# Kernel tuning notes

Hardware: AMD Instinct MI355X
Metric: run time of the kernel (lower is better)

## Reference

```python
import jax, jax.numpy as jnp
import numpy as np
import math

B, S, D = 1, 4096, 1024
H, DK = 16, 64
WINDOW = 256
GLOBAL = 16


def setup_inputs() -> dict:
    key = jax.random.key(0)
    ks = jax.random.split(key, 8)
    scale = 1.0 / math.sqrt(D)  # xavier-ish scale for projections
    return {
        "query": jax.random.normal(ks[0], (B, S, D), jnp.float32),
        "key": jax.random.normal(ks[1], (B, S, D), jnp.float32),
        "value": jax.random.normal(ks[2], (B, S, D), jnp.float32),
        "Wq": jax.random.normal(ks[3], (D, D), jnp.float32) * scale,
        "bq": jnp.zeros((D,), jnp.float32),
        "Wk": jax.random.normal(ks[4], (D, D), jnp.float32) * scale,
        "bk": jnp.zeros((D,), jnp.float32),
        "Wv": jax.random.normal(ks[5], (D, D), jnp.float32) * scale,
        "bv": jnp.zeros((D,), jnp.float32),
        "Wo": jax.random.normal(ks[6], (D, D), jnp.float32) * scale,
        "bo": jnp.zeros((D,), jnp.float32),
    }


def _split_heads(x):
    # [B, S, D] -> [B, H, S, DK]
    return x.reshape(B, S, H, DK).transpose(0, 2, 1, 3)


def reference(query, key, value, Wq, bq, Wk, bk, Wv, bv, Wo, bo):
    Q = _split_heads(query @ Wq + bq)   # [B,H,S,DK]
    K = _split_heads(key @ Wk + bk)
    V = _split_heads(value @ Wv + bv)

    scores = jnp.einsum("bhqd,bhkd->bhqk", Q, K) / math.sqrt(DK)  # [B,H,S,S]

    i = jnp.arange(S)[:, None]
    j = jnp.arange(S)[None, :]
    local = jnp.abs(i - j) <= WINDOW
    glob = (i < GLOBAL) | (j < GLOBAL)
    causal = j <= i
    mask = (local | glob) & causal  # [S,S]

    scores = jnp.where(mask[None, None], scores, -jnp.inf)
    probs = jax.nn.softmax(scores, axis=-1)  # dropout is identity (p=0 / eval)

    out = jnp.einsum("bhqk,bhkd->bhqd", probs, V)  # [B,H,S,DK]
    out = out.transpose(0, 2, 1, 3).reshape(B, S, D)
    return out @ Wo + bo
```

## Files before the change

### kernel.cpp

```cpp
#include <hip/hip_runtime.h>

typedef __bf16 bf16_t;
typedef __attribute__((ext_vector_type(8))) __bf16 bf16x8;
typedef __attribute__((ext_vector_type(4))) __bf16 bf16x4;
typedef __attribute__((ext_vector_type(2))) __bf16 bf16x2;
typedef __attribute__((ext_vector_type(4))) float f32x4;

#define S_LEN 4096
#define D_MODEL 1024
#define NH 16
#define DKH 64
#define WIN 256
#define NGLOB 16
#define HSZ (S_LEN * DKH)

__device__ inline void g2l16(const void* g, void* l) {
  __builtin_amdgcn_global_load_lds(
      (__attribute__((address_space(1))) void*)(void*)g,
      (__attribute__((address_space(3))) void*)l, 16, 0, 0);
}

#define GEMM_BODY(A, Bt)                                                      \
  __shared__ bf16_t As[128 * 32];                                             \
  __shared__ bf16_t Bs[128 * 32];                                             \
  const int tid = threadIdx.x;                                                \
  const int wave = tid >> 6, lane = tid & 63;                                 \
  const int wr = wave >> 1, wc = wave & 1;                                    \
  f32x4 acc[4][4];                                                            \
  _Pragma("unroll") for (int i = 0; i < 4; i++) _Pragma("unroll")             \
      for (int j = 0; j < 4; j++) acc[i][j] = {0.f, 0.f, 0.f, 0.f};          \
  const int srow = lane >> 2;                                                 \
  const int scol = (lane & 3) * 8;                                            \
  const int fr = lane & 15;                                                   \
  const int fk = (lane >> 4) * 8;                                             \
  for (int k0 = 0; k0 < D_MODEL; k0 += 32) {                                  \
    _Pragma("unroll") for (int i = 0; i < 2; i++) {                           \
      const int c = wave * 2 + i;                                             \
      const int row = c * 16 + srow;                                          \
      g2l16(A + (size_t)(m0 + row) * D_MODEL + k0 + scol, &As[c * 512]);      \
      g2l16(Bt + (size_t)(n0 + row) * D_MODEL + k0 + scol, &Bs[c * 512]);     \
    }                                                                         \
    __syncthreads();                                                          \
    bf16x8 af[4], bfr[4];                                                     \
    _Pragma("unroll") for (int m = 0; m < 4; m++) af[m] =                     \
        *(const bf16x8*)&As[(wr * 64 + m * 16 + fr) * 32 + fk];               \
    _Pragma("unroll") for (int n = 0; n < 4; n++) bfr[n] =                    \
        *(const bf16x8*)&Bs[(wc * 64 + n * 16 + fr) * 32 + fk];               \
    _Pragma("unroll") for (int m = 0; m < 4; m++) _Pragma("unroll")           \
        for (int n = 0; n < 4; n++) acc[m][n] =                               \
            __builtin_amdgcn_mfma_f32_16x16x32_bf16(af[m], bfr[n],            \
                                                    acc[m][n], 0, 0, 0);      \
    __syncthreads();                                                          \
  }                                                                           \
  const int cr = (lane >> 4) * 4;                                             \
  const int cc = lane & 15;

__global__ __launch_bounds__(256) void gemm_qkv(
    const bf16_t* __restrict__ Xq, const bf16_t* __restrict__ Xk,
    const bf16_t* __restrict__ Xv, const bf16_t* __restrict__ Wt,
    const float* __restrict__ bq, const float* __restrict__ bk,
    const float* __restrict__ bv, bf16_t* __restrict__ Qo,
    bf16_t* __restrict__ Ko, bf16_t* __restrict__ Vto) {
  const int which = blockIdx.z;
  const bf16_t* A = which == 0 ? Xq : which == 1 ? Xk : Xv;
  const bf16_t* Bt = Wt + (size_t)which * (D_MODEL * D_MODEL);
  const float* bias = which == 0 ? bq : which == 1 ? bk : bv;
  const int m0 = blockIdx.y * 128, n0 = blockIdx.x * 128;

  GEMM_BODY(A, Bt)

#pragma unroll
  for (int m = 0; m < 4; m++) {
    const int rowg = m0 + wr * 64 + m * 16 + cr;
#pragma unroll
    for (int n = 0; n < 4; n++) {
      const int colg = n0 + wc * 64 + n * 16 + cc;
      const float bv_ = bias[colg];
      const int h = colg >> 6, d = colg & 63;
#pragma unroll
      for (int r = 0; r < 4; r++) {
        const int s = rowg + r;
        const float v = acc[m][n][r] + bv_;
        if (which == 0)
          Qo[h * HSZ + s * DKH + d] = (bf16_t)(v * 0.125f);
        else if (which == 1)
          Ko[h * HSZ + s * DKH + d] = (bf16_t)v;
        else
          Vto[h * HSZ + d * S_LEN + s] = (bf16_t)v;
      }
    }
  }
}

__global__ __launch_bounds__(256) void gemm_out(const bf16_t* __restrict__ A_,
                                                const bf16_t* __restrict__ Bt_,
                                                const float* __restrict__ bias,
                                                float* __restrict__ Cout) {
  const int m0 = blockIdx.y * 128, n0 = blockIdx.x * 128;
  GEMM_BODY(A_, Bt_)
#pragma unroll
  for (int m = 0; m < 4; m++) {
    const int rowg = m0 + wr * 64 + m * 16 + cr;
#pragma unroll
    for (int n = 0; n < 4; n++) {
      const int colg = n0 + wc * 64 + n * 16 + cc;
      const float bv_ = bias[colg];
#pragma unroll
      for (int r = 0; r < 4; r++)
        Cout[(size_t)(rowg + r) * D_MODEL + colg] = acc[m][n][r] + bv_;
    }
  }
}

__global__ void convx3(const float* __restrict__ q, const float* __restrict__ k,
                       const float* __restrict__ v, bf16_t* __restrict__ oq,
                       bf16_t* __restrict__ ok, bf16_t* __restrict__ ov) {
  const float* in = blockIdx.y == 0 ? q : blockIdx.y == 1 ? k : v;
  bf16_t* out = blockIdx.y == 0 ? oq : blockIdx.y == 1 ? ok : ov;
  const int i = (blockIdx.x * 256 + threadIdx.x) * 4;
  const float4 x = *(const float4*)&in[i];
  bf16x4 o = {(bf16_t)x.x, (bf16_t)x.y, (bf16_t)x.z, (bf16_t)x.w};
  *(bf16x4*)&out[i] = o;
}

__global__ void convw(const float* __restrict__ W0, const float* __restrict__ W1,
                      const float* __restrict__ W2, const float* __restrict__ W3,
                      bf16_t* __restrict__ out) {
  __shared__ float t[64][65];
  const float* W = blockIdx.z == 0 ? W0 : blockIdx.z == 1 ? W1
                  : blockIdx.z == 2 ? W2 : W3;
  bf16_t* Wt = out + (size_t)blockIdx.z * (D_MODEL * D_MODEL);
  const int k0 = blockIdx.y * 64, n0 = blockIdx.x * 64;
  const int tx = threadIdx.x & 63, ty = threadIdx.x >> 6;
#pragma unroll
  for (int i = 0; i < 16; i++) {
    const int r = i * 4 + ty;
    t[r][tx] = W[(size_t)(k0 + r) * D_MODEL + n0 + tx];
  }
  __syncthreads();
#pragma unroll
  for (int i = 0; i < 16; i++) {
    const int r = i * 4 + ty;
    Wt[(size_t)(n0 + r) * D_MODEL + k0 + tx] = (bf16_t)t[tx][r];
  }
}

__global__ __launch_bounds__(256) void attn_kern(const bf16_t* __restrict__ Q,
                                                 const bf16_t* __restrict__ K,
                                                 const bf16_t* __restrict__ V,
                                                 bf16_t* __restrict__ O) {
  __shared__ bf16_t p_lds[4][16 * 40];
  const int wave = threadIdx.x >> 6, lane = threadIdx.x & 63;
  const int h = blockIdx.y;
  const int q0 = blockIdx.x * 64 + wave * 16;
  const bf16_t* Qh = Q + h * HSZ;
  const bf16_t* Kh = K + h * HSZ;
  const bf16_t* Vh = V + h * HSZ;

  const int fr = lane & 15;
  const int fk = (lane >> 4) * 8;
  const int cr = (lane >> 4) * 4;

  const bf16x8 aq0 = *(const bf16x8*)&Qh[(q0 + fr) * DKH + fk];
  const bf16x8 aq1 = *(const bf16x8*)&Qh[(q0 + fr) * DKH + 32 + fk];

  f32x4 acc_o[4];
#pragma unroll
  for (int i = 0; i < 4; i++) acc_o[i] = {0.f, 0.f, 0.f, 0.f};
  float m_run = -1e30f, l_run = 0.f;

  const int kt_end = (q0 + 15) >> 5;
  int kt_lo = (q0 - WIN) >> 5;
  if (kt_lo < 0) kt_lo = 0;
  const int nt = kt_end - kt_lo + 1 + (kt_lo > 0 ? 1 : 0);

#define TILE_KB(t) ((kt_lo > 0) ? ((t) == 0 ? 0 : (kt_lo + (t)-1) * 32) : (t)*32)
#define LOADK(kb, A0, A1, A2, A3)                              \
  A0 = *(const bf16x8*)&Kh[((kb) + fr) * DKH + fk];            \
  A1 = *(const bf16x8*)&Kh[((kb) + fr) * DKH + 32 + fk];       \
  A2 = *(const bf16x8*)&Kh[((kb) + 16 + fr) * DKH + fk];       \
  A3 = *(const bf16x8*)&Kh[((kb) + 16 + fr) * DKH + 32 + fk];

  bf16x8 kc0, kc1, kc2, kc3;
  {
    const int kb0 = TILE_KB(0);
    LOADK(kb0, kc0, kc1, kc2, kc3)
  }

  const int iq = q0 + fr;
  bf16_t* prow = &p_lds[wave][fr * 40];
  const bf16x8* pread = (const bf16x8*)&p_lds[wave][fr * 40 + fk];

  for (int t = 0; t < nt; t++) {
    const int kb = TILE_KB(t);
    bf16x8 kn0, kn1, kn2, kn3;
    const bool have_next = (t + 1 < nt);
    if (have_next) {
      const int nkb = TILE_KB(t + 1);
      LOADK(nkb, kn0, kn1, kn2, kn3)
    }
    bf16x8 vf0 = *(const bf16x8*)&Vh[(0 * 16 + fr) * S_LEN + kb + fk];
    bf16x8 vf1 = *(const bf16x8*)&Vh[(1 * 16 + fr) * S_LEN + kb + fk];
    bf16x8 vf2 = *(const bf16x8*)&Vh[(2 * 16 + fr) * S_LEN + kb + fk];
    bf16x8 vf3 = *(const bf16x8*)&Vh[(3 * 16 + fr) * S_LEN + kb + fk];

    f32x4 s0 = {0.f, 0.f, 0.f, 0.f}, s1 = {0.f, 0.f, 0.f, 0.f};
    s0 = __builtin_amdgcn_mfma_f32_16x16x32_bf16(kc0, aq0, s0, 0, 0, 0);
    s0 = __builtin_amdgcn_mfma_f32_16x16x32_bf16(kc1, aq1, s0, 0, 0, 0);
    s1 = __builtin_amdgcn_mfma_f32_16x16x32_bf16(kc2, aq0, s1, 0, 0, 0);
    s1 = __builtin_amdgcn_mfma_f32_16x16x32_bf16(kc3, aq1, s1, 0, 0, 0);

    float v[8];
#pragma unroll
    for (int r = 0; r < 4; r++) {
      const int j0 = kb + cr + r, j1 = j0 + 16;
      v[r] = (j0 <= iq && (iq - j0 <= WIN || j0 < NGLOB)) ? s0[r] : -1e30f;
      v[4 + r] = (j1 <= iq && (iq - j1 <= WIN || j1 < NGLOB)) ? s1[r] : -1e30f;
    }
    float mt = fmaxf(fmaxf(fmaxf(v[0], v[1]), fmaxf(v[2], v[3])),
                     fmaxf(fmaxf(v[4], v[5]), fmaxf(v[6], v[7])));
    mt = fmaxf(mt, __shfl_xor(mt, 16));
    mt = fmaxf(mt, __shfl_xor(mt, 32));
    const float mn = fmaxf(m_run, mt);
    const float alpha = __expf(m_run - mn);
    m_run = mn;
    float p[8];
    float ps = 0.f;
#pragma unroll
    for (int i = 0; i < 8; i++) {
      p[i] = __expf(v[i] - mn);
      ps += p[i];
    }
    ps += __shfl_xor(ps, 16);
    ps += __shfl_xor(ps, 32);
    l_run = l_run * alpha + ps;

    *(bf16x2*)&prow[cr] = bf16x2{(bf16_t)p[0], (bf16_t)p[1]};
    *(bf16x2*)&prow[cr + 2] = bf16x2{(bf16_t)p[2], (bf16_t)p[3]};
    *(bf16x2*)&prow[16 + cr] = bf16x2{(bf16_t)p[4], (bf16_t)p[5]};
    *(bf16x2*)&prow[16 + cr + 2] = bf16x2{(bf16_t)p[6], (bf16_t)p[7]};

    float alpha_r[4];
#pragma unroll
    for (int r = 0; r < 4; r++) alpha_r[r] = __shfl(alpha, cr + r);

    asm volatile("" ::: "memory");
    const bf16x8 pa = *pread;
    asm volatile("" ::: "memory");

#pragma unroll
    for (int fd = 0; fd < 4; fd++) {
#pragma unroll
      for (int r = 0; r < 4; r++) acc_o[fd][r] *= alpha_r[r];
    }
    acc_o[0] = __builtin_amdgcn_mfma_f32_16x16x32_bf16(pa, vf0, acc_o[0], 0, 0, 0);
    acc_o[1] = __builtin_amdgcn_mfma_f32_16x16x32_bf16(pa, vf1, acc_o[1], 0, 0, 0);
    acc_o[2] = __builtin_amdgcn_mfma_f32_16x16x32_bf16(pa, vf2, acc_o[2], 0, 0, 0);
    acc_o[3] = __builtin_amdgcn_mfma_f32_16x16x32_bf16(pa, vf3, acc_o[3], 0, 0, 0);

    if (have_next) {
      kc0 = kn0; kc1 = kn1; kc2 = kn2; kc3 = kn3;
    }
  }

  const float linv = 1.0f / l_run;
  float inv_r[4];
#pragma unroll
  for (int r = 0; r < 4; r++) inv_r[r] = __shfl(linv, cr + r);

#pragma unroll
  for (int fd = 0; fd < 4; fd++)
#pragma unroll
    for (int r = 0; r < 4; r++) {
      const int s = q0 + cr + r;
      O[(size_t)s * D_MODEL + h * DKH + fd * 16 + fr] =
          (bf16_t)(acc_o[fd][r] * inv_r[r]);
    }
}

extern "C" void kernel_launch(void* const* d_in, const int* in_sizes, int n_in,
                              void* d_out, int out_size, void* d_ws,
                              size_t ws_size, hipStream_t stream) {
  const float* query = (const float*)d_in[0];
  const float* key = (const float*)d_in[1];
  const float* value = (const float*)d_in[2];
  const float* Wq = (const float*)d_in[3];
  const float* bq = (const float*)d_in[4];
  const float* Wk = (const float*)d_in[5];
  const float* bk = (const float*)d_in[6];
  const float* Wv = (const float*)d_in[7];
  const float* bv = (const float*)d_in[8];
  const float* Wo = (const float*)d_in[9];
  const float* bo = (const float*)d_in[10];

  char* ws = (char*)d_ws;
  bf16_t* Qb = (bf16_t*)(ws);
  bf16_t* Kb = (bf16_t*)(ws + (8ull << 20));
  bf16_t* Vtb = (bf16_t*)(ws + (16ull << 20));
  bf16_t* Wt = (bf16_t*)(ws + (24ull << 20));
  bf16_t* Xq = (bf16_t*)(ws + (32ull << 20));
  bf16_t* Xk = (bf16_t*)(ws + (40ull << 20));
  bf16_t* Xv = (bf16_t*)(ws + (48ull << 20));
  bf16_t* Ab = (bf16_t*)(ws + (56ull << 20));

  const size_t WSTRIDE = (size_t)D_MODEL * D_MODEL;

  convw<<<dim3(16, 16, 4), 256, 0, stream>>>(Wq, Wk, Wv, Wo, Wt);
  convx3<<<dim3(4096, 3), 256, 0, stream>>>(query, key, value, Xq, Xk, Xv);

  gemm_qkv<<<dim3(8, 32, 3), 256, 0, stream>>>(Xq, Xk, Xv, Wt, bq, bk, bv, Qb,
                                               Kb, Vtb);

  attn_kern<<<dim3(64, 16), 256, 0, stream>>>(Qb, Kb, Vtb, Ab);

  gemm_out<<<dim3(8, 32), 256, 0, stream>>>(Ab, Wt + 3 * WSTRIDE, bo,
                                            (float*)d_out);
}
```

Baseline: 130.3 us.

## Double GEMM K-tile to 64, XOR-swizzle LDS, and remap blocks for XCD locality

The shared GEMM body now stages a 64-wide K slice per iteration instead of 32, which halves the number of barrier pairs per tile. An XOR swizzle on the 16-byte column groups avoids LDS bank conflicts when waves read MFMA fragments. Both GEMM grids become 1D, with a block-index remap that places neighbouring tiles on the same XCD to improve L2 reuse of A and B tiles. LDS use per block doubles, which could lower occupancy.

```diff
diff --git a/kernel.cpp b/kernel.cpp
--- a/kernel.cpp
+++ b/kernel.cpp
@@ -21,35 +21,43 @@
 }
 
 #define GEMM_BODY(A, Bt)                                                      \
-  __shared__ bf16_t As[128 * 32];                                             \
-  __shared__ bf16_t Bs[128 * 32];                                             \
+  __shared__ bf16_t As[128 * 64];                                             \
+  __shared__ bf16_t Bs[128 * 64];                                             \
   const int tid = threadIdx.x;                                                \
   const int wave = tid >> 6, lane = tid & 63;                                 \
   const int wr = wave >> 1, wc = wave & 1;                                    \
   f32x4 acc[4][4];                                                            \
   _Pragma("unroll") for (int i = 0; i < 4; i++) _Pragma("unroll")             \
       for (int j = 0; j < 4; j++) acc[i][j] = {0.f, 0.f, 0.f, 0.f};          \
-  const int srow = lane >> 2;                                                 \
-  const int scol = (lane & 3) * 8;                                            \
+  const int srow = lane >> 3;                    \
+  const int scg = lane & 7;                           \
+  const int ssrc = ((scg ^ srow) << 3);     \
   const int fr = lane & 15;                                                   \
-  const int fk = (lane >> 4) * 8;                                             \
-  for (int k0 = 0; k0 < D_MODEL; k0 += 32) {                                  \
-    _Pragma("unroll") for (int i = 0; i < 2; i++) {                           \
-      const int c = wave * 2 + i;                                             \
-      const int row = c * 16 + srow;                                          \
-      g2l16(A + (size_t)(m0 + row) * D_MODEL + k0 + scol, &As[c * 512]);      \
-      g2l16(Bt + (size_t)(n0 + row) * D_MODEL + k0 + scol, &Bs[c * 512]);     \
+  const int fkg = lane >> 4;                                        \
+  for (int k0 = 0; k0 < D_MODEL; k0 += 64) {                                  \
+    _Pragma("unroll") for (int i = 0; i < 4; i++) {                           \
+      const int c = wave * 4 + i;         \
+      const int row = c * 8 + srow;                                           \
+      g2l16(A + (size_t)(m0 + row) * D_MODEL + k0 + ssrc, &As[c * 512]);      \
+      g2l16(Bt + (size_t)(n0 + row) * D_MODEL + k0 + ssrc, &Bs[c * 512]);     \
     }                                                                         \
     __syncthreads();                                                          \
-    bf16x8 af[4], bfr[4];                                                     \
-    _Pragma("unroll") for (int m = 0; m < 4; m++) af[m] =                     \
-        *(const bf16x8*)&As[(wr * 64 + m * 16 + fr) * 32 + fk];               \
-    _Pragma("unroll") for (int n = 0; n < 4; n++) bfr[n] =                    \
-        *(const bf16x8*)&Bs[(wc * 64 + n * 16 + fr) * 32 + fk];               \
-    _Pragma("unroll") for (int m = 0; m < 4; m++) _Pragma("unroll")           \
-        for (int n = 0; n < 4; n++) acc[m][n] =                               \
-            __builtin_amdgcn_mfma_f32_16x16x32_bf16(af[m], bfr[n],            \
-                                                    acc[m][n], 0, 0, 0);      \
+    _Pragma("unroll") for (int kk = 0; kk < 2; kk++) {                        \
+      bf16x8 af[4], bfr[4];                                                   \
+      const int cgs = kk * 4 + fkg;                                           \
+      _Pragma("unroll") for (int m = 0; m < 4; m++) {                         \
+        const int rr = wr * 64 + m * 16 + fr;                                 \
+        af[m] = *(const bf16x8*)&As[rr * 64 + ((cgs ^ (fr & 7)) << 3)];       \
+      }                                                                       \
+      _Pragma("unroll") for (int n = 0; n < 4; n++) {                         \
+        const int rr = wc * 64 + n * 16 + fr;                                 \
+        bfr[n] = *(const bf16x8*)&Bs[rr * 64 + ((cgs ^ (fr & 7)) << 3)];      \
+      }                                                                       \
+      _Pragma("unroll") for (int m = 0; m < 4; m++) _Pragma("unroll")         \
+          for (int n = 0; n < 4; n++) acc[m][n] =                             \
+              __builtin_amdgcn_mfma_f32_16x16x32_bf16(af[m], bfr[n],          \
+                                                      acc[m][n], 0, 0, 0);    \
+    }                                                                         \
     __syncthreads();                                                          \
   }                                                                           \
   const int cr = (lane >> 4) * 4;                                             \
@@ -61,11 +69,15 @@
     const float* __restrict__ bq, const float* __restrict__ bk,
     const float* __restrict__ bv, bf16_t* __restrict__ Qo,
     bf16_t* __restrict__ Ko, bf16_t* __restrict__ Vto) {
-  const int which = blockIdx.z;
+  const int lin = blockIdx.x;
+  const int wg = ((lin & 7) * 96) + (lin >> 3);
+  const int n0 = (wg & 7) * 128;
+  const int m0 = ((wg >> 3) & 31) * 128;
+  const int which = wg >> 8;
+
   const bf16_t* A = which == 0 ? Xq : which == 1 ? Xk : Xv;
   const bf16_t* Bt = Wt + (size_t)which * (D_MODEL * D_MODEL);
   const float* bias = which == 0 ? bq : which == 1 ? bk : bv;
-  const int m0 = blockIdx.y * 128, n0 = blockIdx.x * 128;
 
   GEMM_BODY(A, Bt)
 
@@ -96,7 +108,10 @@
                                                 const bf16_t* __restrict__ Bt_,
                                                 const float* __restrict__ bias,
                                                 float* __restrict__ Cout) {
-  const int m0 = blockIdx.y * 128, n0 = blockIdx.x * 128;
+  const int lin = blockIdx.x;
+  const int wg = ((lin & 7) * 32) + (lin >> 3);
+  const int n0 = (wg & 7) * 128;
+  const int m0 = (wg >> 3) * 128;
   GEMM_BODY(A_, Bt_)
 #pragma unroll
   for (int m = 0; m < 4; m++) {
@@ -308,11 +323,9 @@
   convw<<<dim3(16, 16, 4), 256, 0, stream>>>(Wq, Wk, Wv, Wo, Wt);
   convx3<<<dim3(4096, 3), 256, 0, stream>>>(query, key, value, Xq, Xk, Xv);
 
-  gemm_qkv<<<dim3(8, 32, 3), 256, 0, stream>>>(Xq, Xk, Xv, Wt, bq, bk, bv, Qb,
-                                               Kb, Vtb);
+  gemm_qkv<<<768, 256, 0, stream>>>(Xq, Xk, Xv, Wt, bq, bk, bv, Qb, Kb, Vtb);
 
   attn_kern<<<dim3(64, 16), 256, 0, stream>>>(Qb, Kb, Vtb, Ab);
 
-  gemm_out<<<dim3(8, 32), 256, 0, stream>>>(Ab, Wt + 3 * WSTRIDE, bo,
-                                            (float*)d_out);
-}
+  gemm_out<<<256, 256, 0, stream>>>(Ab, Wt + 3 * WSTRIDE, bo, (float*)d_out);
+}
```

Result: slower. 141.1 us (+8.3%).

## Swizzle GEMM LDS tiles and remap workgroups across XCDs for L2 locality

Applied to the files above, without the earlier changes.

Changes the LDS layout of the GEMM A/B tiles to an XOR-swizzled pairing of rows so the bf16x8 fragment reads avoid bank conflicts. The global_load_lds lanes are permuted to match this layout. Both GEMM kernels also switch to a 1D grid and remap block ids so that consecutive tiles land on the same XCD, aiming for better L2 reuse of shared A/B panels. The index arithmetic is heavier, and a wrong swizzle would silently corrupt results.

```diff
diff --git a/kernel.cpp b/kernel.cpp
--- a/kernel.cpp
+++ b/kernel.cpp
@@ -29,23 +29,37 @@
   f32x4 acc[4][4];                                                            \
   _Pragma("unroll") for (int i = 0; i < 4; i++) _Pragma("unroll")             \
       for (int j = 0; j < 4; j++) acc[i][j] = {0.f, 0.f, 0.f, 0.f};          \
-  const int srow = lane >> 2;                                                 \
-  const int scol = (lane & 3) * 8;                                            \
+     \
+     \
+  const int ssl = (lane & 7) ^ (lane >> 3);                                   \
+  const int srow = 2 * (lane >> 3) + (ssl >> 2);                              \
+  const int scol = 8 * (ssl & 3);                                             \
   const int fr = lane & 15;                                                   \
-  const int fk = (lane >> 4) * 8;                                             \
+  const int fkg = lane >> 4;                             \
   for (int k0 = 0; k0 < D_MODEL; k0 += 32) {                                  \
     _Pragma("unroll") for (int i = 0; i < 2; i++) {                           \
-      const int c = wave * 2 + i;                                             \
-      const int row = c * 16 + srow;                                          \
-      g2l16(A + (size_t)(m0 + row) * D_MODEL + k0 + scol, &As[c * 512]);      \
-      g2l16(Bt + (size_t)(n0 + row) * D_MODEL + k0 + scol, &Bs[c * 512]);     \
+      const int c = wave * 2 + i;                             \
+      const int row0 = c * 16;                                                \
+      g2l16(A + (size_t)(m0 + row0 + srow) * D_MODEL + k0 + scol,             \
+            &As[c * 512]);                                                    \
+      g2l16(Bt + (size_t)(n0 + row0 + srow) * D_MODEL + k0 + scol,            \
+            &Bs[c * 512]);                                                    \
     }                                                                         \
     __syncthreads();                                                          \
     bf16x8 af[4], bfr[4];                                                     \
-    _Pragma("unroll") for (int m = 0; m < 4; m++) af[m] =                     \
-        *(const bf16x8*)&As[(wr * 64 + m * 16 + fr) * 32 + fk];               \
-    _Pragma("unroll") for (int n = 0; n < 4; n++) bfr[n] =                    \
-        *(const bf16x8*)&Bs[(wc * 64 + n * 16 + fr) * 32 + fk];               \
+    _Pragma("unroll") for (int m = 0; m < 4; m++) {                           \
+      const int rr = wr * 64 + m * 16 + fr;                                   \
+      af[m] = *(const bf16x8*)&As[(rr >> 1) * 64 +                            \
+                                  ((((rr & 1) << 2) + fkg) ^ ((rr >> 1) & 7)) \
+                                      * 8];                                   \
+    }                                                                         \
+    _Pragma("unroll") for (int n = 0; n < 4; n++) {                           \
+      const int rr = wc * 64 + n * 16 + fr;                                   \
+      bfr[n] = *(const bf16x8*)&Bs[(rr >> 1) * 64 +                           \
+                                   ((((rr & 1) << 2) + fkg) ^                 \
+                                    ((rr >> 1) & 7)) *                        \
+                                       8];                                    \
+    }                                                                         \
     _Pragma("unroll") for (int m = 0; m < 4; m++) _Pragma("unroll")           \
         for (int n = 0; n < 4; n++) acc[m][n] =                               \
             __builtin_amdgcn_mfma_f32_16x16x32_bf16(af[m], bfr[n],            \
@@ -61,11 +75,15 @@
     const float* __restrict__ bq, const float* __restrict__ bk,
     const float* __restrict__ bv, bf16_t* __restrict__ Qo,
     bf16_t* __restrict__ Ko, bf16_t* __restrict__ Vto) {
-  const int which = blockIdx.z;
+  const int lin = blockIdx.x;
+  const int wg = ((lin & 7) * 96) + (lin >> 3);
+  const int n0 = (wg & 7) * 128;
+  const int m0 = ((wg >> 3) & 31) * 128;
+  const int which = wg >> 8;
+
   const bf16_t* A = which == 0 ? Xq : which == 1 ? Xk : Xv;
   const bf16_t* Bt = Wt + (size_t)which * (D_MODEL * D_MODEL);
   const float* bias = which == 0 ? bq : which == 1 ? bk : bv;
-  const int m0 = blockIdx.y * 128, n0 = blockIdx.x * 128;
 
   GEMM_BODY(A, Bt)
 
@@ -96,7 +114,10 @@
                                                 const bf16_t* __restrict__ Bt_,
                                                 const float* __restrict__ bias,
                                                 float* __restrict__ Cout) {
-  const int m0 = blockIdx.y * 128, n0 = blockIdx.x * 128;
+  const int lin = blockIdx.x;
+  const int wg = ((lin & 7) * 32) + (lin >> 3);
+  const int n0 = (wg & 7) * 128;
+  const int m0 = (wg >> 3) * 128;
   GEMM_BODY(A_, Bt_)
 #pragma unroll
   for (int m = 0; m < 4; m++) {
@@ -308,11 +329,9 @@
   convw<<<dim3(16, 16, 4), 256, 0, stream>>>(Wq, Wk, Wv, Wo, Wt);
   convx3<<<dim3(4096, 3), 256, 0, stream>>>(query, key, value, Xq, Xk, Xv);
 
-  gemm_qkv<<<dim3(8, 32, 3), 256, 0, stream>>>(Xq, Xk, Xv, Wt, bq, bk, bv, Qb,
-                                               Kb, Vtb);
+  gemm_qkv<<<768, 256, 0, stream>>>(Xq, Xk, Xv, Wt, bq, bk, bv, Qb, Kb, Vtb);
 
   attn_kern<<<dim3(64, 16), 256, 0, stream>>>(Qb, Kb, Vtb, Ab);
 
-  gemm_out<<<dim3(8, 32), 256, 0, stream>>>(Ab, Wt + 3 * WSTRIDE, bo,
-                                            (float*)d_out);
-}
+  gemm_out<<<256, 256, 0, stream>>>(Ab, Wt + 3 * WSTRIDE, bo, (float*)d_out);
+}
```

After: 134.4 us. +3.2%, slower.

## Shrink GEMM tiles to 64x128, swizzle LDS layout, remap blocks for XCD locality

Applied to the files above, without the earlier changes.

The QKV and output projection GEMMs now use 64x128 tiles instead of 128x128, doubling the block count (1536 and 512) to fill more CUs. LDS staging uses an XOR-swizzled layout so fragment reads avoid bank conflicts. A linear block index is remapped so consecutive blocks on the same XCD share A/B tiles for L2 reuse. Smaller tiles lower arithmetic intensity per block and add more global traffic for the weight operand.

```diff
diff --git a/kernel.cpp b/kernel.cpp
--- a/kernel.cpp
+++ b/kernel.cpp
@@ -20,40 +20,60 @@
       (__attribute__((address_space(3))) void*)l, 16, 0, 0);
 }
 
-#define GEMM_BODY(A, Bt)                                                      \
-  __shared__ bf16_t As[128 * 32];                                             \
-  __shared__ bf16_t Bs[128 * 32];                                             \
-  const int tid = threadIdx.x;                                                \
-  const int wave = tid >> 6, lane = tid & 63;                                 \
-  const int wr = wave >> 1, wc = wave & 1;                                    \
-  f32x4 acc[4][4];                                                            \
-  _Pragma("unroll") for (int i = 0; i < 4; i++) _Pragma("unroll")             \
-      for (int j = 0; j < 4; j++) acc[i][j] = {0.f, 0.f, 0.f, 0.f};          \
-  const int srow = lane >> 2;                                                 \
-  const int scol = (lane & 3) * 8;                                            \
-  const int fr = lane & 15;                                                   \
-  const int fk = (lane >> 4) * 8;                                             \
-  for (int k0 = 0; k0 < D_MODEL; k0 += 32) {                                  \
-    _Pragma("unroll") for (int i = 0; i < 2; i++) {                           \
-      const int c = wave * 2 + i;                                             \
-      const int row = c * 16 + srow;                                          \
-      g2l16(A + (size_t)(m0 + row) * D_MODEL + k0 + scol, &As[c * 512]);      \
-      g2l16(Bt + (size_t)(n0 + row) * D_MODEL + k0 + scol, &Bs[c * 512]);     \
-    }                                                                         \
-    __syncthreads();                                                          \
-    bf16x8 af[4], bfr[4];                                                     \
-    _Pragma("unroll") for (int m = 0; m < 4; m++) af[m] =                     \
-        *(const bf16x8*)&As[(wr * 64 + m * 16 + fr) * 32 + fk];               \
-    _Pragma("unroll") for (int n = 0; n < 4; n++) bfr[n] =                    \
-        *(const bf16x8*)&Bs[(wc * 64 + n * 16 + fr) * 32 + fk];               \
-    _Pragma("unroll") for (int m = 0; m < 4; m++) _Pragma("unroll")           \
-        for (int n = 0; n < 4; n++) acc[m][n] =                               \
-            __builtin_amdgcn_mfma_f32_16x16x32_bf16(af[m], bfr[n],            \
-                                                    acc[m][n], 0, 0, 0);      \
-    __syncthreads();                                                          \
-  }                                                                           \
-  const int cr = (lane >> 4) * 4;                                             \
-  const int cc = lane & 15;
+template <int DUMMY>
+__device__ __forceinline__ void gemm_body(const bf16_t* __restrict__ A,
+                                          const bf16_t* __restrict__ Bt,
+                                          int m0, int n0, int wave, int lane,
+                                          bf16_t* As, bf16_t* Bs,
+                                          f32x4 acc[2][4]) {
+  const int wr = wave >> 1, wc = wave & 1;
+#pragma unroll
+  for (int i = 0; i < 2; i++)
+#pragma unroll
+    for (int j = 0; j < 4; j++) acc[i][j] = {0.f, 0.f, 0.f, 0.f};
+  const int ssl = (lane & 7) ^ (lane >> 3);
+  const int srow = 2 * (lane >> 3) + (ssl >> 2);
+  const int scol = 8 * (ssl & 3);
+  const int fr = lane & 15;
+  const int fkg = lane >> 4;
+
+  for (int k0 = 0; k0 < D_MODEL; k0 += 32) {
+    {
+      const int row0 = wave * 16;
+      g2l16(A + (size_t)(m0 + row0 + srow) * D_MODEL + k0 + scol,
+            &As[wave * 512]);
+    }
+#pragma unroll
+    for (int i = 0; i < 2; i++) {
+      const int c = wave * 2 + i;
+      g2l16(Bt + (size_t)(n0 + c * 16 + srow) * D_MODEL + k0 + scol,
+            &Bs[c * 512]);
+    }
+    __syncthreads();
+    bf16x8 af[2], bfr[4];
+#pragma unroll
+    for (int m = 0; m < 2; m++) {
+      const int rr = wr * 32 + m * 16 + fr;
+      af[m] = *(const bf16x8*)&As[(rr >> 1) * 64 +
+                                  ((((rr & 1) << 2) + fkg) ^ ((rr >> 1) & 7)) *
+                                      8];
+    }
+#pragma unroll
+    for (int n = 0; n < 4; n++) {
+      const int rr = wc * 64 + n * 16 + fr;
+      bfr[n] = *(const bf16x8*)&Bs[(rr >> 1) * 64 +
+                                   ((((rr & 1) << 2) + fkg) ^ ((rr >> 1) & 7)) *
+                                       8];
+    }
+#pragma unroll
+    for (int m = 0; m < 2; m++)
+#pragma unroll
+      for (int n = 0; n < 4; n++)
+        acc[m][n] = __builtin_amdgcn_mfma_f32_16x16x32_bf16(af[m], bfr[n],
+                                                            acc[m][n], 0, 0, 0);
+    __syncthreads();
+  }
+}
 
 __global__ __launch_bounds__(256) void gemm_qkv(
     const bf16_t* __restrict__ Xq, const bf16_t* __restrict__ Xk,
@@ -61,17 +81,28 @@
     const float* __restrict__ bq, const float* __restrict__ bk,
     const float* __restrict__ bv, bf16_t* __restrict__ Qo,
     bf16_t* __restrict__ Ko, bf16_t* __restrict__ Vto) {
-  const int which = blockIdx.z;
+  __shared__ bf16_t As[64 * 32];
+  __shared__ bf16_t Bs[128 * 32];
+  const int lin = blockIdx.x;
+  const int wg = ((lin & 7) * 192) + (lin >> 3);
+  const int n0 = (wg & 7) * 128;
+  const int m0 = ((wg >> 3) & 63) * 64;
+  const int which = wg >> 9;
+
   const bf16_t* A = which == 0 ? Xq : which == 1 ? Xk : Xv;
   const bf16_t* Bt = Wt + (size_t)which * (D_MODEL * D_MODEL);
   const float* bias = which == 0 ? bq : which == 1 ? bk : bv;
-  const int m0 = blockIdx.y * 128, n0 = blockIdx.x * 128;
-
-  GEMM_BODY(A, Bt)
-
-#pragma unroll
-  for (int m = 0; m < 4; m++) {
-    const int rowg = m0 + wr * 64 + m * 16 + cr;
+
+  const int wave = threadIdx.x >> 6, lane = threadIdx.x & 63;
+  f32x4 acc[2][4];
+  gemm_body<0>(A, Bt, m0, n0, wave, lane, As, Bs, acc);
+
+  const int wr = wave >> 1, wc = wave & 1;
+  const int cr = (lane >> 4) * 4;
+  const int cc = lane & 15;
+#pragma unroll
+  for (int m = 0; m < 2; m++) {
+    const int rowg = m0 + wr * 32 + m * 16 + cr;
 #pragma unroll
     for (int n = 0; n < 4; n++) {
       const int colg = n0 + wc * 64 + n * 16 + cc;
@@ -96,11 +127,22 @@
                                                 const bf16_t* __restrict__ Bt_,
                                                 const float* __restrict__ bias,
                                                 float* __restrict__ Cout) {
-  const int m0 = blockIdx.y * 128, n0 = blockIdx.x * 128;
-  GEMM_BODY(A_, Bt_)
-#pragma unroll
-  for (int m = 0; m < 4; m++) {
-    const int rowg = m0 + wr * 64 + m * 16 + cr;
+  __shared__ bf16_t As[64 * 32];
+  __shared__ bf16_t Bs[128 * 32];
+  const int lin = blockIdx.x;
+  const int wg = ((lin & 7) * 64) + (lin >> 3);
+  const int n0 = (wg & 7) * 128;
+  const int m0 = (wg >> 3) * 64;
+  const int wave = threadIdx.x >> 6, lane = threadIdx.x & 63;
+  f32x4 acc[2][4];
+  gemm_body<0>(A_, Bt_, m0, n0, wave, lane, As, Bs, acc);
+
+  const int wr = wave >> 1, wc = wave & 1;
+  const int cr = (lane >> 4) * 4;
+  const int cc = lane & 15;
+#pragma unroll
+  for (int m = 0; m < 2; m++) {
+    const int rowg = m0 + wr * 32 + m * 16 + cr;
 #pragma unroll
     for (int n = 0; n < 4; n++) {
       const int colg = n0 + wc * 64 + n * 16 + cc;
@@ -308,11 +350,9 @@
   convw<<<dim3(16, 16, 4), 256, 0, stream>>>(Wq, Wk, Wv, Wo, Wt);
   convx3<<<dim3(4096, 3), 256, 0, stream>>>(query, key, value, Xq, Xk, Xv);
 
-  gemm_qkv<<<dim3(8, 32, 3), 256, 0, stream>>>(Xq, Xk, Xv, Wt, bq, bk, bv, Qb,
-                                               Kb, Vtb);
+  gemm_qkv<<<1536, 256, 0, stream>>>(Xq, Xk, Xv, Wt, bq, bk, bv, Qb, Kb, Vtb);
 
   attn_kern<<<dim3(64, 16), 256, 0, stream>>>(Qb, Kb, Vtb, Ab);
 
-  gemm_out<<<dim3(8, 32), 256, 0, stream>>>(Ab, Wt + 3 * WSTRIDE, bo,
-                                            (float*)d_out);
-}
+  gemm_out<<<512, 256, 0, stream>>>(Ab, Wt + 3 * WSTRIDE, bo, (float*)d_out);
+}
```

After: 139.6 us. 7.2% more time.
